# Kernel tuning notes

Hardware: AMD Instinct MI355X
Metric: run time of the kernel (lower is better)

## Reference

```python
import jax, jax.numpy as jnp
import numpy as np


def _dconv(x, W, b, d):
    # dilated 3x3 conv, padding=d so spatial size is preserved (NCHW / OIHW)
    y = jax.lax.conv_general_dilated(
        x, W, window_strides=(1, 1), padding=((d, d), (d, d)),
        rhs_dilation=(d, d), dimension_numbers=('NCHW', 'OIHW', 'NCHW'))
    return y + b[None, :, None, None]


def setup_inputs() -> dict:
    key = jax.random.key(0)
    ks = jax.random.split(key, 12)
    B, C, H, W = 2, 512, 64, 64
    s = 0.02  # keep pre-softmax energies in a sane range
    inp = {
        'x':  jax.random.normal(ks[0], (B, C, H, W), jnp.float32),
        'W1': jax.random.normal(ks[1], (128, 512, 3, 3), jnp.float32) * s,
        'b1': jnp.zeros((128,), jnp.float32),
        'W2': jax.random.normal(ks[2], (128, 512, 3, 3), jnp.float32) * s,
        'b2': jnp.zeros((128,), jnp.float32),
        'W3': jax.random.normal(ks[3], (128, 512, 3, 3), jnp.float32) * s,
        'b3': jnp.zeros((128,), jnp.float32),
        'W4': jax.random.normal(ks[4], (128, 512, 3, 3), jnp.float32) * s,
        'b4': jnp.zeros((128,), jnp.float32),
        'Wd':  jax.random.normal(ks[5], (512, 128), jnp.float32) * s,   # dense, 1x1 no bias
        'Wcc': jax.random.normal(ks[6], (256, 512), jnp.float32) * s,   # CCIFL conv 512->256
        'bcc': jnp.zeros((256,), jnp.float32),
        'Wd2': jax.random.normal(ks[7], (512, 256), jnp.float32) * s,   # dense2, 1x1 no bias
    }
    return inp


def reference(x, W1, b1, W2, b2, W3, b3, W4, b4, Wd, Wcc, bcc, Wd2):
    B, C, H, W = x.shape
    N = H * W
    # four dilated-conv feature maps, flattened to [B, 128, N]
    a1 = jax.nn.relu(_dconv(x, W1, b1, 2)).reshape(B, 128, N)
    a2 = jax.nn.relu(_dconv(x, W2, b2, 3)).reshape(B, 128, N)
    a3 = jax.nn.relu(_dconv(x, W3, b3, 5)).reshape(B, 128, N)
    a4 = jax.nn.relu(_dconv(x, W4, b4, 7)).reshape(B, 128, N)

    # spatial attention 1: softmax(a1^T a2), applied as a4 @ att
    att12 = jax.nn.softmax(jnp.einsum('bcn,bcm->bnm', a1, a2), axis=-1)
    o1 = jnp.einsum('bcn,bnm->bcm', a4, att12).reshape(B, 128, H, W)
    o1 = jnp.einsum('oc,bchw->bohw', Wd, o1)  # dense 128->512

    # spatial attention 2: softmax(a3^T a4), applied as a2 @ att
    att34 = jax.nn.softmax(jnp.einsum('bcn,bcm->bnm', a3, a4), axis=-1)
    o2 = jnp.einsum('bcn,bnm->bcm', a2, att34).reshape(B, 128, H, W)
    o2 = jnp.einsum('oc,bchw->bohw', Wd, o2)

    def ccifl(y):
        # GAP -> 1x1 conv (512->256) -> scalar qk attention (softmax over a 1x1 -> 1)
        g = jnp.mean(y, axis=(2, 3))                        # [B, 512]
        z = jnp.einsum('oc,bc->bo', Wcc, g) + bcc           # [B, 256]
        e = jnp.einsum('bc,bc->b', z, z)[:, None, None]     # [B, 1, 1]
        att = jax.nn.softmax(e, axis=-1)                    # == 1
        return z * att[:, 0, :]                             # [B, 256]

    c1 = jnp.einsum('oc,bc->bo', Wd2, ccifl(o1))            # [B, 512]
    c2 = jnp.einsum('oc,bc->bo', Wd2, ccifl(o2))
    # broadcast [B,512,1,1] channel attention over spatial dims + residual
    return c1[:, :, None, None] + c2[:, :, None, None] + x
```

## Files before the change

kernel.cpp:

```cpp
#include <hip/hip_runtime.h>
#include <hip/hip_bf16.h>

typedef short short8 __attribute__((ext_vector_type(8)));
typedef float f32x4 __attribute__((ext_vector_type(4)));
typedef unsigned short u16;

#define XT_OFF   0
#define XT_BYTES (2*78*78*512*2)
#define WR2_OFF  (XT_OFF + XT_BYTES)
#define WR2_BYTES (2*9*16*8*64*16)
#define AFTER_W  (WR2_OFF + WR2_BYTES)
#define P_OFF    AFTER_W
#define P_BYTES  (4*4*4096*128*2)
#define GA_OFF_P (P_OFF + P_BYTES)
#define CA_OFF   AFTER_W
#define CA_BYTES (4*4096*128*4)
#define GA_OFF_A (CA_OFF + CA_BYTES)
#define GA_BYTES 2048
#define GV_REL   GA_BYTES
#define ZV_REL   (GV_REL + 4*512*4)
#define TAIL_END (ZV_REL + 4*256*4)
#define WS_NEED_P ((size_t)GA_OFF_P + TAIL_END)
#define WS_NEED_A ((size_t)GA_OFF_A + TAIL_END)

static __device__ __forceinline__ void async_cp16(u16* lds, const u16* g) {
  __builtin_amdgcn_global_load_lds(
      (const __attribute__((address_space(1))) void*)g,
      (__attribute__((address_space(3))) void*)lds, 16, 0, 0);
}

__global__ void zero_u4(uint4* __restrict__ p, int n) {
  int i = blockIdx.x * blockDim.x + threadIdx.x;
  int st = gridDim.x * blockDim.x;
  uint4 z = {0u, 0u, 0u, 0u};
  for (; i < n; i += st) p[i] = z;
}

__global__ void prep_all(const float* __restrict__ x, u16* __restrict__ xT,
                         const float* __restrict__ W2, const float* __restrict__ W4,
                         u16* __restrict__ Wr2, float* __restrict__ gapacc) {
  int bid = blockIdx.x;
  int t = threadIdx.x;
  if (bid < 1024) {
    __shared__ float tile[64][65];
    int bh = bid >> 3, cc = bid & 7;
    int b = bh >> 6, h = bh & 63;
    int w = t & 63, cq4 = t >> 6;
    int pi = t >> 2, q = t & 3;
#pragma unroll
    for (int i = 0; i < 16; ++i) {
      int ci = cq4 + i * 4;
      tile[ci][w] = x[((b * 512 + cc * 64 + ci) * 4096) + h * 64 + w];
    }
    __syncthreads();
    union { u16 u[16]; uint4 v[2]; } pk;
#pragma unroll
    for (int k = 0; k < 16; ++k) {
      __hip_bfloat16 hb = __float2bfloat16(tile[q * 16 + k][pi]);
      pk.u[k] = *(u16*)&hb;
    }
    u16* dst = xT + ((size_t)(b * 78 + h + 7) * 78 + (pi + 7)) * 512 + cc * 64 + q * 16;
    *(uint4*)dst = pk.v[0];
    *(uint4*)(dst + 8) = pk.v[1];
  } else if (bid < 1312) {
    int hb = bid - 1024;
    size_t off; int cnt;
    if (hb < 256) {
      int b = hb >> 7, rem = hb & 127, h = rem >> 1, side = rem & 1;
      off = ((size_t)(b * 78 + 7 + h) * 78 + (side ? 71 : 0)) * 512;
      cnt = 7 * 512;
    } else {
      int k = hb - 256;
      int b = k >> 4, topbot = (k >> 3) & 1, ch = k & 7;
      off = ((size_t)b * 78 + (topbot ? 71 : 0)) * 78 * 512 + (size_t)ch * 34944;
      cnt = 34944;
    }
    uint4* p = (uint4*)(xT + off);
    int n = cnt >> 3;
    uint4 z = {0u, 0u, 0u, 0u};
    for (int i = t; i < n; i += blockDim.x) p[i] = z;
  } else if (bid < 1568) {
    int idx = bid - 1312;
    int conv = idx >> 7, o = idx & 127;
    const float* W = conv ? W4 : W2;
    __shared__ float sw[4608];
    const float* src = W + (size_t)o * 4608;
    for (int k = 0; k < 18; ++k) sw[t + k * 256] = src[t + k * 256];
    __syncthreads();
    if (t < 144) {
      int tap = t >> 4, kc = t & 15;
      int wn = o >> 6, ni = (o >> 4) & 3;
      size_t base = (size_t)conv * 589824 + (size_t)(tap * 16 + kc) * 4096
                    + (wn * 4 + ni) * 512;
#pragma unroll
      for (int cg = 0; cg < 4; ++cg) {
        union { u16 h[8]; uint4 v; } pk;
#pragma unroll
        for (int e = 0; e < 8; ++e) {
          __hip_bfloat16 hb = __float2bfloat16(sw[(kc * 32 + cg * 8 + e) * 9 + tap]);
          pk.h[e] = *(u16*)&hb;
        }
        int lane = cg * 16 + (o & 15);
        *(uint4*)(Wr2 + base + lane * 8) = pk.v;
      }
    }
  } else {
    gapacc[t] = 0.f;
    gapacc[t + 256] = 0.f;
  }
}

template<int MODE>
__global__ __launch_bounds__(256, 2) void conv_mfma(
    const u16* __restrict__ xT, const u16* __restrict__ Wr2,
    u16* __restrict__ Pp, float* __restrict__ convacc) {
  __shared__ __align__(16) u16 Ab[2][8192];
  int bid = blockIdx.x;
  int xcd = bid & 7, cq = (bid >> 3) & 3, conv = (bid >> 5) & 1;
  int pthi = (bid >> 6) & 3, b = bid >> 8;
  int pt = pthi * 8 + xcd;
  int u = conv * 2 + b;
  int d = conv ? 7 : 3;
  int h0 = pt * 2;
  const u16* xb = xT + (size_t)b * (78 * 78 * 512);
  int t = threadIdx.x, l = t & 63, wv = t >> 6;

  int slog = (l & 7) ^ (l >> 3);
  int wq = wv * 8 + (l >> 3);
  const u16* gA[4];
#pragma unroll
  for (int m = 0; m < 4; ++m) {
    int hh = m >> 1, mh = m & 1;
    gA[m] = xb + ((size_t)(h0 + hh - d + 7) * 78 + (mh * 32 + wq - d + 7)) * 512
            + cq * 128 + slog * 8;
  }
  const char* bB = (const char*)Wr2 + (size_t)conv * 1179648
                   + cq * 32768 + wv * 2048 + l * 16;

  int rbase = (l & 15) * 64;
  int rs0 = (((l >> 4)) ^ (l & 7)) * 8;
  int rs1 = ((4 + (l >> 4)) ^ (l & 7)) * 8;

  f32x4 acc[8][2];
#pragma unroll
  for (int i = 0; i < 8; ++i)
#pragma unroll
    for (int jj = 0; jj < 2; ++jj) acc[i][jj] = (f32x4){0.f, 0.f, 0.f, 0.f};

  short8 bf0[2][2], bf1[2][2];

  auto issueA = [&](int buf) {
#pragma unroll
    for (int m = 0; m < 4; ++m)
      async_cp16(&Ab[buf][m * 2048 + wv * 512], gA[m]);
    __builtin_amdgcn_sched_barrier(0);
  };
  auto loadB = [&](short8 bf[2][2]) {
#pragma unroll
    for (int c01 = 0; c01 < 2; ++c01)
#pragma unroll
      for (int ni = 0; ni < 2; ++ni)
        bf[c01][ni] = *(const short8*)(bB + c01 * 8192 + ni * 1024);
  };
  auto cbar = [&]() {
    __builtin_amdgcn_sched_barrier(0);
    asm volatile("s_waitcnt vmcnt(4)" ::: "memory");
    __builtin_amdgcn_s_barrier();
    __builtin_amdgcn_sched_barrier(0);
  };
  auto advance = [&](int s) {
    int dA, dB;
    if (!(s & 1)) { dA = 64; dB = 16384; }
    else {
      dB = 114688;
      int tap = (s + 1) >> 1;
      dA = (tap % 3) ? (512 * d - 64) : (38912 * d - 64);
    }
#pragma unroll
    for (int m = 0; m < 4; ++m) gA[m] += dA;
    bB += dB;
  };
  auto compute = [&](int buf, short8 bf[2][2]) {
    const u16* A = Ab[buf];
#pragma unroll
    for (int mi = 0; mi < 8; ++mi) {
      short8 a0 = *(const short8*)&A[rbase + mi * 1024 + rs0];
      short8 a1 = *(const short8*)&A[rbase + mi * 1024 + rs1];
      acc[mi][0] = __builtin_amdgcn_mfma_f32_16x16x32_bf16(a0, bf[0][0], acc[mi][0], 0, 0, 0);
      acc[mi][1] = __builtin_amdgcn_mfma_f32_16x16x32_bf16(a0, bf[0][1], acc[mi][1], 0, 0, 0);
      acc[mi][0] = __builtin_amdgcn_mfma_f32_16x16x32_bf16(a1, bf[1][0], acc[mi][0], 0, 0, 0);
      acc[mi][1] = __builtin_amdgcn_mfma_f32_16x16x32_bf16(a1, bf[1][1], acc[mi][1], 0, 0, 0);
    }
  };

  issueA(0); loadB(bf0); advance(0);
  cbar();
  for (int it = 0; it < 9; ++it) {
    int s = it * 2;
    issueA(1); loadB(bf1); advance(s + 1);
    compute(0, bf0);
    cbar();
    if (it < 8) { issueA(0); loadB(bf0); advance(s + 2); }
    compute(1, bf1);
    cbar();
  }

  if (MODE == 0) {
    u16* PP = Pp + ((size_t)(cq * 4 + u) * 4096 + pt * 128 + (l >> 4) * 4) * 128
              + wv * 32 + (l & 15);
#pragma unroll
    for (int mi = 0; mi < 8; ++mi)
#pragma unroll
      for (int ni = 0; ni < 2; ++ni)
#pragma unroll
        for (int jj = 0; jj < 4; ++jj) {
          __hip_bfloat16 hv = __float2bfloat16(acc[mi][ni][jj]);
          PP[(mi * 16 + jj) * 128 + ni * 16] = *(u16*)&hv;
        }
  } else {
    float* ca = convacc + (size_t)u * 4096 * 128;
#pragma unroll
    for (int mi = 0; mi < 8; ++mi)
#pragma unroll
      for (int ni = 0; ni < 2; ++ni)
#pragma unroll
        for (int jj = 0; jj < 4; ++jj) {
          int pos = pt * 128 + mi * 16 + (l >> 4) * 4 + jj;
          int oc = wv * 32 + ni * 16 + (l & 15);
          atomicAdd(&ca[pos * 128 + oc], acc[mi][ni][jj]);
        }
  }
}

__global__ void reduce_gap_p(const u16* __restrict__ P,
                             const float* __restrict__ b2, const float* __restrict__ b4,
                             float* __restrict__ gapacc) {
  int u = blockIdx.x >> 6, g = blockIdx.x & 63;
  int conv = u >> 1;
  const float* bias = conv ? b4 : b2;
  int t = threadIdx.x;
  int oct = (t & 15) * 8, pl = t >> 4;
  float bi[8];
  *(float4*)&bi[0] = *(const float4*)&bias[oct];
  *(float4*)&bi[4] = *(const float4*)&bias[oct + 4];
  float s[8];
#pragma unroll
  for (int e = 0; e < 8; ++e) s[e] = 0.f;
  for (int i = 0; i < 4; ++i) {
    int pos = g * 64 + pl * 4 + i;
    size_t base = ((size_t)u * 4096 + pos) * 128 + oct;
    float v[8];
#pragma unroll
    for (int e = 0; e < 8; ++e) v[e] = bi[e];
#pragma unroll
    for (int cq = 0; cq < 4; ++cq) {
      uint4 q = *(const uint4*)&P[base + (size_t)cq * 2097152];
      unsigned w[4] = {q.x, q.y, q.z, q.w};
#pragma unroll
      for (int k = 0; k < 4; ++k) {
        v[k * 2]     += __builtin_bit_cast(float, (w[k] & 0xffffu) << 16);
        v[k * 2 + 1] += __builtin_bit_cast(float, w[k] & 0xffff0000u);
      }
    }
#pragma unroll
    for (int e = 0; e < 8; ++e) s[e] += v[e] > 0.f ? v[e] : 0.f;
  }
  __shared__ float red[16][128];
#pragma unroll
  for (int e = 0; e < 8; ++e) red[pl][oct + e] = s[e];
  __syncthreads();
  if (t < 128) {
    float acc = 0.f;
#pragma unroll
    for (int r = 0; r < 16; ++r) acc += red[r][t];
    atomicAdd(&gapacc[u * 128 + t], acc);
  }
}

__global__ void reduce_gap_a(const float* __restrict__ convacc,
                             const float* __restrict__ b2, const float* __restrict__ b4,
                             float* __restrict__ gapacc) {
  int unit = blockIdx.x >> 5, chunk = blockIdx.x & 31;
  int conv = unit >> 1;
  const float* bias = conv ? b4 : b2;
  int t = threadIdx.x, oc = t & 127, half = t >> 7;
  const float* ca = convacc + (size_t)unit * 4096 * 128;
  float bi = bias[oc];
  float s = 0.f;
  for (int i = 0; i < 64; ++i) {
    int pos = chunk * 128 + half * 64 + i;
    float v = ca[pos * 128 + oc] + bi;
    s += v > 0.f ? v : 0.f;
  }
  __shared__ float red[2][128];
  red[half][oc] = s;
  __syncthreads();
  if (t < 128) atomicAdd(&gapacc[unit * 128 + t], red[0][t] + red[1][t]);
}

__global__ void dense1(const float* __restrict__ gapacc, const float* __restrict__ Wd,
                       float* __restrict__ gv) {
  int o = blockIdx.x, t = threadIdx.x;
  float w = Wd[o * 128 + t];
  float p0 = w * gapacc[2 * 128 + t];
  float p1 = w * gapacc[0 * 128 + t];
  float p2 = w * gapacc[3 * 128 + t];
  float p3 = w * gapacc[1 * 128 + t];
#pragma unroll
  for (int m = 1; m < 64; m <<= 1) {
    p0 += __shfl_xor(p0, m); p1 += __shfl_xor(p1, m);
    p2 += __shfl_xor(p2, m); p3 += __shfl_xor(p3, m);
  }
  __shared__ float red[2][4];
  if ((t & 63) == 0) {
    red[t >> 6][0] = p0; red[t >> 6][1] = p1;
    red[t >> 6][2] = p2; red[t >> 6][3] = p3;
  }
  __syncthreads();
  if (t < 4) {
    const float inv = 1.f / 4096.f;
    gv[t * 512 + o] = (red[0][t] + red[1][t]) * inv;
  }
}

__global__ void dense2(const float* __restrict__ gv, const float* __restrict__ Wcc,
                       const float* __restrict__ bcc, float* __restrict__ zv) {
  int o = blockIdx.x, t = threadIdx.x;
  float w0 = Wcc[o * 512 + t], w1 = Wcc[o * 512 + 256 + t];
  float p[4];
#pragma unroll
  for (int c = 0; c < 4; ++c)
    p[c] = w0 * gv[c * 512 + t] + w1 * gv[c * 512 + 256 + t];
#pragma unroll
  for (int m = 1; m < 64; m <<= 1)
#pragma unroll
    for (int c = 0; c < 4; ++c) p[c] += __shfl_xor(p[c], m);
  __shared__ float red[4][4];
  if ((t & 63) == 0)
#pragma unroll
    for (int c = 0; c < 4; ++c) red[t >> 6][c] = p[c];
  __syncthreads();
  if (t < 4) {
    float s = bcc[o];
#pragma unroll
    for (int wv = 0; wv < 4; ++wv) s += red[wv][t];
    zv[t * 256 + o] = s;
  }
}

__global__ void final_add(const float* __restrict__ x, const float* __restrict__ zv,
                          const float* __restrict__ Wd2, float* __restrict__ out) {
  int t = threadIdx.x, bid = blockIdx.x;
  int ch = (bid >> 2) & 511;
  float w = Wd2[ch * 256 + t];
  float p0 = w * (zv[t] + zv[256 + t]);
  float p1 = w * (zv[512 + t] + zv[768 + t]);
#pragma unroll
  for (int m = 1; m < 64; m <<= 1) {
    p0 += __shfl_xor(p0, m);
    p1 += __shfl_xor(p1, m);
  }
  __shared__ float red[4][2];
  __shared__ float cv[2];
  if ((t & 63) == 0) { red[t >> 6][0] = p0; red[t >> 6][1] = p1; }
  __syncthreads();
  if (t < 2) cv[t] = red[0][t] + red[1][t] + red[2][t] + red[3][t];
  __syncthreads();
  const float4* x4 = (const float4*)x;
  float4* o4 = (float4*)out;
  int i = bid * 256 + t;
  float c0 = cv[0], c1 = cv[1];
  float4 v = x4[i];
  v.x += c0; v.y += c0; v.z += c0; v.w += c0;
  o4[i] = v;
  i += 524288;
  float4 v2 = x4[i];
  v2.x += c1; v2.y += c1; v2.z += c1; v2.w += c1;
  o4[i] = v2;
}

extern "C" void kernel_launch(void* const* d_in, const int* in_sizes, int n_in,
                              void* d_out, int out_size, void* d_ws, size_t ws_size,
                              hipStream_t stream) {
  const float* x   = (const float*)d_in[0];
  const float* W2  = (const float*)d_in[3];
  const float* b2  = (const float*)d_in[4];
  const float* W4  = (const float*)d_in[7];
  const float* b4  = (const float*)d_in[8];
  const float* Wd  = (const float*)d_in[9];
  const float* Wcc = (const float*)d_in[10];
  const float* bcc = (const float*)d_in[11];
  const float* Wd2 = (const float*)d_in[12];
  float* out = (float*)d_out;

  char* ws = (char*)d_ws;
  u16* xT  = (u16*)(ws + XT_OFF);
  u16* Wr2 = (u16*)(ws + WR2_OFF);

  const bool partial = ws_size >= WS_NEED_P;
  size_t ga_off = partial ? GA_OFF_P : GA_OFF_A;
  float* gapacc = (float*)(ws + ga_off);
  float* gv     = (float*)(ws + ga_off + GV_REL);
  float* zv     = (float*)(ws + ga_off + ZV_REL);

  prep_all<<<1569, 256, 0, stream>>>(x, xT, W2, W4, Wr2, gapacc);

  if (partial) {
    u16* Pp = (u16*)(ws + P_OFF);
    conv_mfma<0><<<512, 256, 0, stream>>>(xT, Wr2, Pp, nullptr);
    reduce_gap_p<<<256, 256, 0, stream>>>(Pp, b2, b4, gapacc);
  } else {
    float* convacc = (float*)(ws + CA_OFF);
    zero_u4<<<512, 256, 0, stream>>>((uint4*)convacc, CA_BYTES / 16);
    conv_mfma<1><<<512, 256, 0, stream>>>(xT, Wr2, nullptr, convacc);
    reduce_gap_a<<<128, 256, 0, stream>>>(convacc, b2, b4, gapacc);
  }

  dense1<<<512, 128, 0, stream>>>(gapacc, Wd, gv);
  dense2<<<256, 256, 0, stream>>>(gv, Wcc, bcc, zv);
  final_add<<<2048, 256, 0, stream>>>(x, zv, Wd2, out);
}
```

Baseline: 54.73 us.

## Store conv partials channel-major and reduce GAP per channel without atomics

```diff
diff --git a/kernel.cpp b/kernel.cpp
--- a/kernel.cpp
+++ b/kernel.cpp
@@ -11,7 +11,7 @@
 #define WR2_BYTES (2*9*16*8*64*16)
 #define AFTER_W  (WR2_OFF + WR2_BYTES)
 #define P_OFF    AFTER_W
-#define P_BYTES  (4*4*4096*128*2)
+#define P_BYTES  (4*4*128*4096*2)
 #define GA_OFF_P (P_OFF + P_BYTES)
 #define CA_OFF   AFTER_W
 #define CA_BYTES (4*4096*128*4)
@@ -38,7 +38,7 @@
 
 __global__ void prep_all(const float* __restrict__ x, u16* __restrict__ xT,
                          const float* __restrict__ W2, const float* __restrict__ W4,
-                         u16* __restrict__ Wr2, float* __restrict__ gapacc) {
+                         u16* __restrict__ Wr2) {
   int bid = blockIdx.x;
   int t = threadIdx.x;
   if (bid < 1024) {
@@ -79,7 +79,7 @@
     int n = cnt >> 3;
     uint4 z = {0u, 0u, 0u, 0u};
     for (int i = t; i < n; i += blockDim.x) p[i] = z;
-  } else if (bid < 1568) {
+  } else {
     int idx = bid - 1312;
     int conv = idx >> 7, o = idx & 127;
     const float* W = conv ? W4 : W2;
@@ -104,9 +104,6 @@
         *(uint4*)(Wr2 + base + lane * 8) = pk.v;
       }
     }
-  } else {
-    gapacc[t] = 0.f;
-    gapacc[t + 256] = 0.f;
   }
 }
 
@@ -206,17 +203,21 @@
   }
 
   if (MODE == 0) {
-    u16* PP = Pp + ((size_t)(cq * 4 + u) * 4096 + pt * 128 + (l >> 4) * 4) * 128
-              + wv * 32 + (l & 15);
+    u16* PPt = Pp + ((size_t)(cq * 4 + u) * 128 + wv * 32 + (l & 15)) * 4096
+               + pt * 128 + (l >> 4) * 4;
 #pragma unroll
     for (int mi = 0; mi < 8; ++mi)
 #pragma unroll
-      for (int ni = 0; ni < 2; ++ni)
-#pragma unroll
-        for (int jj = 0; jj < 4; ++jj) {
-          __hip_bfloat16 hv = __float2bfloat16(acc[mi][ni][jj]);
-          PP[(mi * 16 + jj) * 128 + ni * 16] = *(u16*)&hv;
-        }
+      for (int ni = 0; ni < 2; ++ni) {
+        __hip_bfloat16 h0 = __float2bfloat16(acc[mi][ni][0]);
+        __hip_bfloat16 h1 = __float2bfloat16(acc[mi][ni][1]);
+        __hip_bfloat16 h2 = __float2bfloat16(acc[mi][ni][2]);
+        __hip_bfloat16 h3 = __float2bfloat16(acc[mi][ni][3]);
+        uint2 v;
+        v.x = (unsigned)*(u16*)&h0 | ((unsigned)*(u16*)&h1 << 16);
+        v.y = (unsigned)*(u16*)&h2 | ((unsigned)*(u16*)&h3 << 16);
+        *(uint2*)(PPt + (size_t)ni * 65536 + mi * 16) = v;
+      }
   } else {
     float* ca = convacc + (size_t)u * 4096 * 128;
 #pragma unroll
@@ -235,46 +236,35 @@
 __global__ void reduce_gap_p(const u16* __restrict__ P,
                              const float* __restrict__ b2, const float* __restrict__ b4,
                              float* __restrict__ gapacc) {
-  int u = blockIdx.x >> 6, g = blockIdx.x & 63;
-  int conv = u >> 1;
-  const float* bias = conv ? b4 : b2;
+  int u = blockIdx.x >> 7, oc = blockIdx.x & 127;
+  const float* bias = (u >> 1) ? b4 : b2;
   int t = threadIdx.x;
-  int oct = (t & 15) * 8, pl = t >> 4;
-  float bi[8];
-  *(float4*)&bi[0] = *(const float4*)&bias[oct];
-  *(float4*)&bi[4] = *(const float4*)&bias[oct + 4];
-  float s[8];
-#pragma unroll
-  for (int e = 0; e < 8; ++e) s[e] = 0.f;
-  for (int i = 0; i < 4; ++i) {
-    int pos = g * 64 + pl * 4 + i;
-    size_t base = ((size_t)u * 4096 + pos) * 128 + oct;
-    float v[8];
-#pragma unroll
-    for (int e = 0; e < 8; ++e) v[e] = bi[e];
-#pragma unroll
-    for (int cq = 0; cq < 4; ++cq) {
-      uint4 q = *(const uint4*)&P[base + (size_t)cq * 2097152];
-      unsigned w[4] = {q.x, q.y, q.z, q.w};
-#pragma unroll
-      for (int k = 0; k < 4; ++k) {
-        v[k * 2]     += __builtin_bit_cast(float, (w[k] & 0xffffu) << 16);
-        v[k * 2 + 1] += __builtin_bit_cast(float, w[k] & 0xffff0000u);
-      }
-    }
-#pragma unroll
-    for (int e = 0; e < 8; ++e) s[e] += v[e] > 0.f ? v[e] : 0.f;
-  }
-  __shared__ float red[16][128];
-#pragma unroll
-  for (int e = 0; e < 8; ++e) red[pl][oct + e] = s[e];
-  __syncthreads();
-  if (t < 128) {
-    float acc = 0.f;
-#pragma unroll
-    for (int r = 0; r < 16; ++r) acc += red[r][t];
-    atomicAdd(&gapacc[u * 128 + t], acc);
-  }
+  float bi = bias[oc];
+  const u16* p0 = P + ((size_t)u * 128 + oc) * 4096 + t * 16;
+  float v[16];
+#pragma unroll
+  for (int k = 0; k < 16; ++k) v[k] = bi;
+#pragma unroll
+  for (int cq = 0; cq < 4; ++cq) {
+    const u16* pp = p0 + (size_t)cq * 2097152;
+    uint4 a = *(const uint4*)pp;
+    uint4 bq = *(const uint4*)(pp + 8);
+    unsigned w[8] = {a.x, a.y, a.z, a.w, bq.x, bq.y, bq.z, bq.w};
+#pragma unroll
+    for (int k = 0; k < 8; ++k) {
+      v[2 * k]     += __builtin_bit_cast(float, (w[k] & 0xffffu) << 16);
+      v[2 * k + 1] += __builtin_bit_cast(float, w[k] & 0xffff0000u);
+    }
+  }
+  float s = 0.f;
+#pragma unroll
+  for (int k = 0; k < 16; ++k) s += v[k] > 0.f ? v[k] : 0.f;
+#pragma unroll
+  for (int m = 1; m < 64; m <<= 1) s += __shfl_xor(s, m);
+  __shared__ float red[4];
+  if ((t & 63) == 0) red[t >> 6] = s;
+  __syncthreads();
+  if (t == 0) gapacc[u * 128 + oc] = red[0] + red[1] + red[2] + red[3];
 }
 
 __global__ void reduce_gap_a(const float* __restrict__ convacc,
@@ -403,15 +393,15 @@
   float* gv     = (float*)(ws + ga_off + GV_REL);
   float* zv     = (float*)(ws + ga_off + ZV_REL);
 
-  prep_all<<<1569, 256, 0, stream>>>(x, xT, W2, W4, Wr2, gapacc);
+  prep_all<<<1568, 256, 0, stream>>>(x, xT, W2, W4, Wr2);
 
   if (partial) {
     u16* Pp = (u16*)(ws + P_OFF);
     conv_mfma<0><<<512, 256, 0, stream>>>(xT, Wr2, Pp, nullptr);
-    reduce_gap_p<<<256, 256, 0, stream>>>(Pp, b2, b4, gapacc);
+    reduce_gap_p<<<512, 256, 0, stream>>>(Pp, b2, b4, gapacc);
   } else {
     float* convacc = (float*)(ws + CA_OFF);
-    zero_u4<<<512, 256, 0, stream>>>((uint4*)convacc, CA_BYTES / 16);
+    zero_u4<<<512, 256, 0, stream>>>((uint4*)convacc, (CA_BYTES + GA_BYTES) / 16);
     conv_mfma<1><<<512, 256, 0, stream>>>(xT, Wr2, nullptr, convacc);
     reduce_gap_a<<<128, 256, 0, stream>>>(convacc, b2, b4, gapacc);
   }
```

After: 56.95 us. 4.1% more time.
